# Performance work log

Measured on AMD Instinct MI355X. Metric: run time of the kernel, lower is better.

Reference implementation:

```python
import jax, jax.numpy as jnp
import numpy as np

B, N, C = 2, 2048, 1024
H = 16
D = C // H  # head_dim = 64
SCALE = D ** -0.5


def setup_inputs() -> dict:
    key = jax.random.key(0)
    k1, k2, k3, k4 = jax.random.split(key, 4)
    x = jax.random.normal(k1, (B, N, C), dtype=jnp.float32)
    # nn.Linear(in_dim, 3*out_dim, bias=False): store as [in, 3*out] for x @ W
    w_qkv = jax.random.normal(k2, (C, 3 * C), dtype=jnp.float32) * (C ** -0.5)
    w_proj = jax.random.normal(k3, (C, C), dtype=jnp.float32) * (C ** -0.5)
    b_proj = jax.random.normal(k4, (C,), dtype=jnp.float32) * 0.01
    return {"x": x, "w_qkv": w_qkv, "w_proj": w_proj, "b_proj": b_proj}


def reference(x, w_qkv, w_proj, b_proj):
    b, n, c = x.shape
    # QKV projection -> [3, B, H, N, D]
    qkv = (x @ w_qkv).reshape(b, n, 3, H, D).transpose(2, 0, 3, 1, 4)
    q, k, v = qkv[0], qkv[1], qkv[2]
    # scaled dot-product attention, full [B, H, N, N] scores as in original
    attn = jax.nn.softmax(jnp.einsum('bhqd,bhkd->bhqk', q * SCALE, k), axis=-1)
    out = jnp.einsum('bhqk,bhkd->bhqd', attn, v)  # [B, H, N, D]
    out = out.transpose(0, 2, 1, 3).reshape(b, n, c)
    return out @ w_proj + b_proj
```

## Files before the change

kernel.cpp:

```cpp
#include <hip/hip_runtime.h>

typedef unsigned short u16;
typedef float f32x4 __attribute__((ext_vector_type(4)));
typedef short bf16x8 __attribute__((ext_vector_type(8)));
typedef u16 u16x4 __attribute__((ext_vector_type(4)));
typedef u16 u16x8 __attribute__((ext_vector_type(8)));
typedef __bf16 bfr4 __attribute__((ext_vector_type(4)));

#define BB 2
#define NN 2048
#define CC 1024
#define HH 16
#define DD 64
#define MM (BB * NN)
#define NQKV (3 * CC)
#define QSCALE 0.18033688011112042f

#if __has_builtin(__builtin_amdgcn_exp2f)
#define EXP2(x) __builtin_amdgcn_exp2f(x)
#else
#define EXP2(x) exp2f(x)
#endif

__device__ __forceinline__ u16 f2bf(float f) {
    unsigned u = __float_as_uint(f);
    u += 0x7FFFu + ((u >> 16) & 1u);
    return (u16)(u >> 16);
}

__device__ __forceinline__ void ld_lds16(const u16* g, u16* l) {
    __builtin_amdgcn_global_load_lds(
        (const __attribute__((address_space(1))) unsigned int*)g,
        (__attribute__((address_space(3))) unsigned int*)l, 16, 0, 0);
}

__global__ __launch_bounds__(256) void k_prep(const float* __restrict__ x,
                                              const float* __restrict__ wqkv,
                                              const float* __restrict__ wproj,
                                              u16* __restrict__ Xb,
                                              u16* __restrict__ Wq,
                                              u16* __restrict__ Wp) {
    __shared__ float tile[32][33];
    int bid = blockIdx.x, t = threadIdx.x;
    if (bid < 2048) {
        int i = (bid * 256 + t) * 8;
        float4 a = *(const float4*)(x + i);
        float4 b = *(const float4*)(x + i + 4);
        u16x8 o;
        o[0] = f2bf(a.x); o[1] = f2bf(a.y); o[2] = f2bf(a.z); o[3] = f2bf(a.w);
        o[4] = f2bf(b.x); o[5] = f2bf(b.y); o[6] = f2bf(b.z); o[7] = f2bf(b.w);
        *(u16x8*)(Xb + i) = o;
        return;
    }
    const float* in;
    u16* out;
    int Nn, n0, k0;
    if (bid < 2048 + 3072) {
        int b2 = bid - 2048;
        in = wqkv; out = Wq; Nn = NQKV;
        n0 = (b2 % 96) * 32; k0 = (b2 / 96) * 32;
    } else {
        int b3 = bid - 5120;
        in = wproj; out = Wp; Nn = CC;
        n0 = (b3 & 31) * 32; k0 = (b3 >> 5) * 32;
    }
    int tx = t & 31, ty = t >> 5;
#pragma unroll
    for (int r = 0; r < 32; r += 8)
        tile[ty + r][tx] = in[(size_t)(k0 + ty + r) * Nn + n0 + tx];
    __syncthreads();
#pragma unroll
    for (int r = 0; r < 32; r += 8)
        out[(size_t)(n0 + ty + r) * CC + k0 + tx] = f2bf(tile[tx][ty + r]);
}

__global__ __launch_bounds__(512) void k_gemmq(
    const u16* __restrict__ A, const u16* __restrict__ B,
    u16* __restrict__ Qb, u16* __restrict__ Kb, u16* __restrict__ Vb) {
    const int Kd = 1024;
    __shared__ __align__(16) u16 Ah0[256][64], Bh0[256][64];
    __shared__ __align__(16) u16 Ah1[256][64], Bh1[256][64];

    int t = threadIdx.x, wave = t >> 6, lane = t & 63;
    int quad = lane >> 4, l16 = lane & 15;
    int wr = wave >> 2, wc = wave & 3;
    int m0 = blockIdx.y * 256, n0 = blockIdx.x * 256;

    int strow = wave * 8 + (lane >> 3);
    int stdst = (lane & 7) * 8;
    int stsrc = ((lane & 7) ^ (lane >> 3)) * 8;

    f32x4 acc[8][4];
#pragma unroll
    for (int i = 0; i < 8; i++)
#pragma unroll
        for (int j = 0; j < 4; j++) acc[i][j] = f32x4{0.f, 0.f, 0.f, 0.f};

    auto STAGE = [&](int k0, u16 (*Ad)[64], u16 (*Bd)[64]) {
#pragma unroll
        for (int i = 0; i < 4; i++) {
            int row = i * 64 + strow;
            ld_lds16(A + (size_t)(m0 + row) * Kd + k0 + stsrc, &Ad[row][stdst]);
            ld_lds16(B + (size_t)(n0 + row) * Kd + k0 + stsrc, &Bd[row][stdst]);
        }
    };
    auto COMPUTE = [&](u16 (*As)[64], u16 (*Bs)[64]) {
#pragma unroll
        for (int s = 0; s < 2; s++) {
            int pos = ((s * 4 + quad) ^ (l16 & 7)) * 8;
            bf16x8 af[8], bg[4];
#pragma unroll
            for (int m = 0; m < 8; m++)
                af[m] = *(const bf16x8*)&As[wr * 128 + m * 16 + l16][pos];
#pragma unroll
            for (int n = 0; n < 4; n++)
                bg[n] = *(const bf16x8*)&Bs[wc * 64 + n * 16 + l16][pos];
#pragma unroll
            for (int m = 0; m < 8; m++)
#pragma unroll
                for (int n = 0; n < 4; n++)
                    acc[m][n] = __builtin_amdgcn_mfma_f32_16x16x32_bf16(
                        af[m], bg[n], acc[m][n], 0, 0, 0);
        }
    };

    STAGE(0, Ah0, Bh0);
    __syncthreads();
    for (int k0 = 0; k0 < Kd; k0 += 128) {
        STAGE(k0 + 64, Ah1, Bh1);
        COMPUTE(Ah0, Bh0);
        __syncthreads();
        if (k0 + 128 < Kd) STAGE(k0 + 128, Ah0, Bh0);
        COMPUTE(Ah1, Bh1);
        __syncthreads();
    }

#pragma unroll
    for (int m = 0; m < 8; m++)
#pragma unroll
        for (int n = 0; n < 4; n++)
#pragma unroll
            for (int r = 0; r < 4; r++) {
                int grow = m0 + wr * 128 + m * 16 + quad * 4 + r;
                int gcol = n0 + wc * 64 + n * 16 + l16;
                float v = acc[m][n][r];
                int three = gcol >> 10, rem = gcol & 1023;
                int h = rem >> 6, d = rem & 63;
                int bb = grow >> 11, nn = grow & 2047;
                if (three == 0) {
                    Qb[((size_t)(bb * HH + h) * NN + nn) * DD + d] = f2bf(v * QSCALE);
                } else if (three == 1) {
                    Kb[((size_t)(bb * HH + h) * NN + nn) * DD + d] = f2bf(v);
                } else {
                    Vb[((size_t)(bb * HH + h) * DD + d) * NN + nn] = f2bf(v);
                }
            }
}

__global__ __launch_bounds__(256) void k_gemmp(
    const u16* __restrict__ A, const u16* __restrict__ B,
    const float* __restrict__ bias, float* __restrict__ Cout) {
    const int Kd = 1024;
    __shared__ __align__(16) u16 Ah[128][32];
    __shared__ __align__(16) u16 Bh[128][32];

    int t = threadIdx.x;
    int wave = t >> 6, lane = t & 63;
    int quad = lane >> 4, l16 = lane & 15;
    int wm = (wave >> 1) * 64, wn = (wave & 1) * 64;
    int m0 = blockIdx.y * 128, n0 = blockIdx.x * 128;

    int strow0 = wave * 16 + (lane >> 2);
    int stdst  = (lane & 3) * 8;
    int stsrc  = ((lane & 3) ^ ((lane >> 3) & 3)) * 8;
    int cfrag = (quad ^ ((l16 >> 1) & 3)) * 8;

    f32x4 acc[4][4];
#pragma unroll
    for (int i = 0; i < 4; i++)
#pragma unroll
        for (int j = 0; j < 4; j++) acc[i][j] = f32x4{0.f, 0.f, 0.f, 0.f};

    for (int k0 = 0; k0 < Kd; k0 += 32) {
        __syncthreads();
#pragma unroll
        for (int ii = 0; ii < 2; ii++) {
            int row = strow0 + ii * 64;
            ld_lds16(A + (size_t)(m0 + row) * Kd + k0 + stsrc, &Ah[row][stdst]);
            ld_lds16(B + (size_t)(n0 + row) * Kd + k0 + stsrc, &Bh[row][stdst]);
        }
        __syncthreads();

        bf16x8 af[4], bf[4];
#pragma unroll
        for (int i = 0; i < 4; i++) {
            af[i] = *(const bf16x8*)&Ah[wm + i * 16 + l16][cfrag];
            bf[i] = *(const bf16x8*)&Bh[wn + i * 16 + l16][cfrag];
        }
#pragma unroll
        for (int mi = 0; mi < 4; mi++)
#pragma unroll
            for (int ni = 0; ni < 4; ni++)
                acc[mi][ni] = __builtin_amdgcn_mfma_f32_16x16x32_bf16(
                    af[mi], bf[ni], acc[mi][ni], 0, 0, 0);
    }

#pragma unroll
    for (int mi = 0; mi < 4; mi++)
#pragma unroll
        for (int ni = 0; ni < 4; ni++)
#pragma unroll
            for (int r = 0; r < 4; r++) {
                int grow = m0 + wm + mi * 16 + quad * 4 + r;
                int gcol = n0 + wn + ni * 16 + l16;
                Cout[(size_t)grow * CC + gcol] = acc[mi][ni][r] + bias[gcol];
            }
}

__global__ __launch_bounds__(512) void k_attn(const u16* __restrict__ Qb,
                                              const u16* __restrict__ Kb,
                                              const u16* __restrict__ VbT,
                                              u16* __restrict__ Ob) {
    __shared__ __align__(16) u16 Ks0[64][64], Ks1[64][64];
    __shared__ __align__(16) u16 Vs0[64][64], Vs1[64][64];
    __shared__ __align__(16) u16 Ps[8][16][72];

    int t = threadIdx.x, wave = t >> 6, lane = t & 63;
    int quad = lane >> 4, l16 = lane & 15;
    int bh = blockIdx.y, q0 = blockIdx.x * 128;
    const size_t kbase = (size_t)bh * NN * DD;
    const size_t vbase = (size_t)bh * DD * NN;

    int qrow = q0 + wave * 16 + l16;
    bf16x8 qf0 = *(const bf16x8*)&Qb[kbase + (size_t)qrow * DD + quad * 8];
    bf16x8 qf1 = *(const bf16x8*)&Qb[kbase + (size_t)qrow * DD + 32 + quad * 8];

    f32x4 o[4];
#pragma unroll
    for (int i = 0; i < 4; i++) o[i] = f32x4{0.f, 0.f, 0.f, 0.f};
    f32x4 lrow = f32x4{0.f, 0.f, 0.f, 0.f};

    int stgrp = lane & 7;
    int stsrc = (stgrp ^ (lane >> 3)) * 8;
    int strow = wave * 8 + (lane >> 3);
    int cf0 = (quad ^ (l16 & 7)) * 8;
    int cf1 = ((4 + quad) ^ (l16 & 7)) * 8;

    auto STAGE = [&](int cc, u16 (*Kd_)[64], u16 (*Vd_)[64]) {
        ld_lds16(&Kb[kbase + (size_t)(cc * 64 + strow) * DD + stsrc],
                 &Kd_[strow][stgrp * 8]);
        ld_lds16(&VbT[vbase + (size_t)strow * NN + cc * 64 + stsrc],
                 &Vd_[strow][stgrp * 8]);
    };

    auto COMPUTE = [&](u16 (*Ksrc)[64], u16 (*Vsrc)[64]) {
        bf16x8 kf[4][2];
#pragma unroll
        for (int kt = 0; kt < 4; kt++) {
            kf[kt][0] = *(const bf16x8*)&Ksrc[kt * 16 + l16][cf0];
            kf[kt][1] = *(const bf16x8*)&Ksrc[kt * 16 + l16][cf1];
        }
        f32x4 s[4];
        __builtin_amdgcn_s_setprio(1);
#pragma unroll
        for (int kt = 0; kt < 4; kt++) {
            f32x4 z = f32x4{0.f, 0.f, 0.f, 0.f};
            z = __builtin_amdgcn_mfma_f32_16x16x32_bf16(kf[kt][0], qf0, z, 0, 0, 0);
            z = __builtin_amdgcn_mfma_f32_16x16x32_bf16(kf[kt][1], qf1, z, 0, 0, 0);
            s[kt] = z;
        }
        __builtin_amdgcn_s_setprio(0);
#pragma unroll
        for (int kt = 0; kt < 4; kt++) {
            bfr4 pk;
#pragma unroll
            for (int r = 0; r < 4; r++) {
                float e = EXP2(s[kt][r]);
                lrow[r] += e;
                pk[r] = (__bf16)e;
            }
            *(bfr4*)&Ps[wave][l16][kt * 16 + quad * 4] = pk;
        }
        __asm__ volatile("s_waitcnt lgkmcnt(0)" ::: "memory");
        bf16x8 pb0 = *(const bf16x8*)&Ps[wave][l16][quad * 8];
        bf16x8 pb1 = *(const bf16x8*)&Ps[wave][l16][32 + quad * 8];
        __builtin_amdgcn_s_setprio(1);
#pragma unroll
        for (int dt = 0; dt < 4; dt++) {
            bf16x8 vf0 = *(const bf16x8*)&Vsrc[dt * 16 + l16][cf0];
            bf16x8 vf1 = *(const bf16x8*)&Vsrc[dt * 16 + l16][cf1];
            o[dt] = __builtin_amdgcn_mfma_f32_16x16x32_bf16(vf0, pb0, o[dt], 0, 0, 0);
            o[dt] = __builtin_amdgcn_mfma_f32_16x16x32_bf16(vf1, pb1, o[dt], 0, 0, 0);
        }
        __builtin_amdgcn_s_setprio(0);
    };

    STAGE(0, Ks0, Vs0);
    __syncthreads();

    for (int c = 0; c < NN / 64; c += 2) {
        STAGE(c + 1, Ks1, Vs1);
        COMPUTE(Ks0, Vs0);
        __syncthreads();
        if (c + 2 < NN / 64) STAGE(c + 2, Ks0, Vs0);
        COMPUTE(Ks1, Vs1);
        __syncthreads();
    }

    int b = bh >> 4, h = bh & 15;
    float l = (lrow[0] + lrow[1]) + (lrow[2] + lrow[3]);
    l += __shfl_xor(l, 16, 64);
    l += __shfl_xor(l, 32, 64);
    float inv = 1.f / l;
    int grow = b * NN + q0 + wave * 16 + l16;
#pragma unroll
    for (int dt = 0; dt < 4; dt++) {
        u16x4 hv;
#pragma unroll
        for (int r = 0; r < 4; r++) hv[r] = f2bf(o[dt][r] * inv);
        int gcol = h * DD + dt * 16 + quad * 4;
        *(u16x4*)&Ob[(size_t)grow * CC + gcol] = hv;
    }
}

extern "C" void kernel_launch(void* const* d_in, const int* in_sizes, int n_in,
                              void* d_out, int out_size, void* d_ws, size_t ws_size,
                              hipStream_t stream) {
    const float* x      = (const float*)d_in[0];
    const float* w_qkv  = (const float*)d_in[1];
    const float* w_proj = (const float*)d_in[2];
    const float* b_proj = (const float*)d_in[3];
    float* out = (float*)d_out;

    u16* p = (u16*)d_ws;
    u16* Xb = p; p += (size_t)MM * CC;
    u16* Wq = p; p += (size_t)NQKV * CC;
    u16* Wp = p; p += (size_t)CC * CC;
    u16* Qb = p; p += (size_t)MM * CC;
    u16* Kb = p; p += (size_t)MM * CC;
    u16* Vb = p; p += (size_t)MM * CC;
    u16* Ob = p; p += (size_t)MM * CC;

    k_prep<<<2048 + 3072 + 1024, 256, 0, stream>>>(x, w_qkv, w_proj, Xb, Wq, Wp);
    k_gemmq<<<dim3(NQKV / 256, MM / 256), 512, 0, stream>>>(Xb, Wq, Qb, Kb, Vb);
    k_attn<<<dim3(NN / 128, BB * HH), 512, 0, stream>>>(Qb, Kb, Vb, Ob);
    k_gemmp<<<dim3(CC / 128, MM / 128), 256, 0, stream>>>(Ob, Wp, b_proj, out);
}
```

Baseline: 203.4 us.

## Shrink GEMM tiles for more blocks, double-buffer projection GEMM, raise MFMA priority

The QKV GEMM moves from 256x256 to 128x192 tiles, which turns 192 blocks into 512 so the 256 CUs get better occupancy and wave balance. The output-projection GEMM is rewritten from a single-buffered 128x128, K=32 loop into a double-buffered 64x128, K=64 pipeline with the swizzled staging, giving 512 blocks. Both kernels raise wave priority around their MFMA bursts. The cost is lower per-block data reuse, so each block loads more operand bytes from global memory per output.

```diff
diff --git a/kernel.cpp b/kernel.cpp
--- a/kernel.cpp
+++ b/kernel.cpp
@@ -74,33 +74,37 @@
         out[(size_t)(n0 + ty + r) * CC + k0 + tx] = f2bf(tile[tx][ty + r]);
 }
 
-__global__ __launch_bounds__(512) void k_gemmq(
+__global__ __launch_bounds__(512, 4) void k_gemmq(
     const u16* __restrict__ A, const u16* __restrict__ B,
     u16* __restrict__ Qb, u16* __restrict__ Kb, u16* __restrict__ Vb) {
     const int Kd = 1024;
-    __shared__ __align__(16) u16 Ah0[256][64], Bh0[256][64];
-    __shared__ __align__(16) u16 Ah1[256][64], Bh1[256][64];
+    __shared__ __align__(16) u16 Ah0[128][64], Bh0[192][64];
+    __shared__ __align__(16) u16 Ah1[128][64], Bh1[192][64];
 
     int t = threadIdx.x, wave = t >> 6, lane = t & 63;
     int quad = lane >> 4, l16 = lane & 15;
     int wr = wave >> 2, wc = wave & 3;
-    int m0 = blockIdx.y * 256, n0 = blockIdx.x * 256;
+    int m0 = blockIdx.y * 128, n0 = blockIdx.x * 192;
 
     int strow = wave * 8 + (lane >> 3);
     int stdst = (lane & 7) * 8;
     int stsrc = ((lane & 7) ^ (lane >> 3)) * 8;
 
-    f32x4 acc[8][4];
-#pragma unroll
-    for (int i = 0; i < 8; i++)
-#pragma unroll
-        for (int j = 0; j < 4; j++) acc[i][j] = f32x4{0.f, 0.f, 0.f, 0.f};
+    f32x4 acc[4][3];
+#pragma unroll
+    for (int i = 0; i < 4; i++)
+#pragma unroll
+        for (int j = 0; j < 3; j++) acc[i][j] = f32x4{0.f, 0.f, 0.f, 0.f};
 
     auto STAGE = [&](int k0, u16 (*Ad)[64], u16 (*Bd)[64]) {
 #pragma unroll
-        for (int i = 0; i < 4; i++) {
+        for (int i = 0; i < 2; i++) {
             int row = i * 64 + strow;
             ld_lds16(A + (size_t)(m0 + row) * Kd + k0 + stsrc, &Ad[row][stdst]);
+        }
+#pragma unroll
+        for (int i = 0; i < 3; i++) {
+            int row = i * 64 + strow;
             ld_lds16(B + (size_t)(n0 + row) * Kd + k0 + stsrc, &Bd[row][stdst]);
         }
     };
@@ -108,19 +112,21 @@
 #pragma unroll
         for (int s = 0; s < 2; s++) {
             int pos = ((s * 4 + quad) ^ (l16 & 7)) * 8;
-            bf16x8 af[8], bg[4];
-#pragma unroll
-            for (int m = 0; m < 8; m++)
-                af[m] = *(const bf16x8*)&As[wr * 128 + m * 16 + l16][pos];
-#pragma unroll
-            for (int n = 0; n < 4; n++)
-                bg[n] = *(const bf16x8*)&Bs[wc * 64 + n * 16 + l16][pos];
-#pragma unroll
-            for (int m = 0; m < 8; m++)
-#pragma unroll
-                for (int n = 0; n < 4; n++)
+            bf16x8 af[4], bg[3];
+#pragma unroll
+            for (int m = 0; m < 4; m++)
+                af[m] = *(const bf16x8*)&As[wr * 64 + m * 16 + l16][pos];
+#pragma unroll
+            for (int n = 0; n < 3; n++)
+                bg[n] = *(const bf16x8*)&Bs[wc * 48 + n * 16 + l16][pos];
+            __builtin_amdgcn_s_setprio(1);
+#pragma unroll
+            for (int m = 0; m < 4; m++)
+#pragma unroll
+                for (int n = 0; n < 3; n++)
                     acc[m][n] = __builtin_amdgcn_mfma_f32_16x16x32_bf16(
                         af[m], bg[n], acc[m][n], 0, 0, 0);
+            __builtin_amdgcn_s_setprio(0);
         }
     };
 
@@ -136,13 +142,13 @@
     }
 
 #pragma unroll
-    for (int m = 0; m < 8; m++)
-#pragma unroll
-        for (int n = 0; n < 4; n++)
+    for (int m = 0; m < 4; m++)
+#pragma unroll
+        for (int n = 0; n < 3; n++)
 #pragma unroll
             for (int r = 0; r < 4; r++) {
-                int grow = m0 + wr * 128 + m * 16 + quad * 4 + r;
-                int gcol = n0 + wc * 64 + n * 16 + l16;
+                int grow = m0 + wr * 64 + m * 16 + quad * 4 + r;
+                int gcol = n0 + wc * 48 + n * 16 + l16;
                 float v = acc[m][n][r];
                 int three = gcol >> 10, rem = gcol & 1023;
                 int h = rem >> 6, d = rem & 63;
@@ -161,59 +167,77 @@
     const u16* __restrict__ A, const u16* __restrict__ B,
     const float* __restrict__ bias, float* __restrict__ Cout) {
     const int Kd = 1024;
-    __shared__ __align__(16) u16 Ah[128][32];
-    __shared__ __align__(16) u16 Bh[128][32];
-
-    int t = threadIdx.x;
-    int wave = t >> 6, lane = t & 63;
+    __shared__ __align__(16) u16 Ah0[64][64], Bh0[128][64];
+    __shared__ __align__(16) u16 Ah1[64][64], Bh1[128][64];
+
+    int t = threadIdx.x, wave = t >> 6, lane = t & 63;
     int quad = lane >> 4, l16 = lane & 15;
-    int wm = (wave >> 1) * 64, wn = (wave & 1) * 64;
-    int m0 = blockIdx.y * 128, n0 = blockIdx.x * 128;
-
-    int strow0 = wave * 16 + (lane >> 2);
-    int stdst  = (lane & 3) * 8;
-    int stsrc  = ((lane & 3) ^ ((lane >> 3) & 3)) * 8;
-    int cfrag = (quad ^ ((l16 >> 1) & 3)) * 8;
-
-    f32x4 acc[4][4];
+    int m0 = blockIdx.y * 64, n0 = blockIdx.x * 128;
+
+    int strow = wave * 8 + (lane >> 3);
+    int stdst = (lane & 7) * 8;
+    int stsrc = ((lane & 7) ^ (lane >> 3)) * 8;
+
+    f32x4 acc[4][2];
 #pragma unroll
     for (int i = 0; i < 4; i++)
 #pragma unroll
-        for (int j = 0; j < 4; j++) acc[i][j] = f32x4{0.f, 0.f, 0.f, 0.f};
-
-    for (int k0 = 0; k0 < Kd; k0 += 32) {
-        __syncthreads();
-#pragma unroll
-        for (int ii = 0; ii < 2; ii++) {
-            int row = strow0 + ii * 64;
-            ld_lds16(A + (size_t)(m0 + row) * Kd + k0 + stsrc, &Ah[row][stdst]);
-            ld_lds16(B + (size_t)(n0 + row) * Kd + k0 + stsrc, &Bh[row][stdst]);
-        }
-        __syncthreads();
-
-        bf16x8 af[4], bf[4];
+        for (int j = 0; j < 2; j++) acc[i][j] = f32x4{0.f, 0.f, 0.f, 0.f};
+
+    auto STAGE = [&](int k0, u16 (*Ad)[64], u16 (*Bd)[64]) {
+#pragma unroll
+        for (int i = 0; i < 2; i++) {
+            int row = i * 32 + strow;
+            ld_lds16(A + (size_t)(m0 + row) * Kd + k0 + stsrc, &Ad[row][stdst]);
+        }
 #pragma unroll
         for (int i = 0; i < 4; i++) {
-            af[i] = *(const bf16x8*)&Ah[wm + i * 16 + l16][cfrag];
-            bf[i] = *(const bf16x8*)&Bh[wn + i * 16 + l16][cfrag];
-        }
-#pragma unroll
-        for (int mi = 0; mi < 4; mi++)
-#pragma unroll
-            for (int ni = 0; ni < 4; ni++)
-                acc[mi][ni] = __builtin_amdgcn_mfma_f32_16x16x32_bf16(
-                    af[mi], bf[ni], acc[mi][ni], 0, 0, 0);
-    }
-
-#pragma unroll
-    for (int mi = 0; mi < 4; mi++)
-#pragma unroll
-        for (int ni = 0; ni < 4; ni++)
+            int row = i * 32 + strow;
+            ld_lds16(B + (size_t)(n0 + row) * Kd + k0 + stsrc, &Bd[row][stdst]);
+        }
+    };
+    auto COMPUTE = [&](u16 (*As)[64], u16 (*Bs)[64]) {
+#pragma unroll
+        for (int s = 0; s < 2; s++) {
+            int pos = ((s * 4 + quad) ^ (l16 & 7)) * 8;
+            bf16x8 af[4], bg[2];
+#pragma unroll
+            for (int m = 0; m < 4; m++)
+                af[m] = *(const bf16x8*)&As[m * 16 + l16][pos];
+#pragma unroll
+            for (int n = 0; n < 2; n++)
+                bg[n] = *(const bf16x8*)&Bs[wave * 32 + n * 16 + l16][pos];
+            __builtin_amdgcn_s_setprio(1);
+#pragma unroll
+            for (int m = 0; m < 4; m++)
+#pragma unroll
+                for (int n = 0; n < 2; n++)
+                    acc[m][n] = __builtin_amdgcn_mfma_f32_16x16x32_bf16(
+                        af[m], bg[n], acc[m][n], 0, 0, 0);
+            __builtin_amdgcn_s_setprio(0);
+        }
+    };
+
+    STAGE(0, Ah0, Bh0);
+    __syncthreads();
+    for (int k0 = 0; k0 < Kd; k0 += 128) {
+        STAGE(k0 + 64, Ah1, Bh1);
+        COMPUTE(Ah0, Bh0);
+        __syncthreads();
+        if (k0 + 128 < Kd) STAGE(k0 + 128, Ah0, Bh0);
+        COMPUTE(Ah1, Bh1);
+        __syncthreads();
+    }
+
+#pragma unroll
+    for (int m = 0; m < 4; m++)
+#pragma unroll
+        for (int n = 0; n < 2; n++)
 #pragma unroll
             for (int r = 0; r < 4; r++) {
-                int grow = m0 + wm + mi * 16 + quad * 4 + r;
-                int gcol = n0 + wn + ni * 16 + l16;
-                Cout[(size_t)grow * CC + gcol] = acc[mi][ni][r] + bias[gcol];
+                int grow = m0 + m * 16 + quad * 4 + r;
+                int gcol = n0 + wave * 32 + n * 16 + l16;
+                Cout[(size_t)grow * CC + gcol] = acc[m][n][r] + bias[gcol];
             }
 }
 
@@ -342,7 +366,7 @@
     u16* Ob = p; p += (size_t)MM * CC;
 
     k_prep<<<2048 + 3072 + 1024, 256, 0, stream>>>(x, w_qkv, w_proj, Xb, Wq, Wp);
-    k_gemmq<<<dim3(NQKV / 256, MM / 256), 512, 0, stream>>>(Xb, Wq, Qb, Kb, Vb);
+    k_gemmq<<<dim3(NQKV / 192, MM / 128), 512, 0, stream>>>(Xb, Wq, Qb, Kb, Vb);
     k_attn<<<dim3(NN / 128, BB * HH), 512, 0, stream>>>(Qb, Kb, Vb, Ob);
-    k_gemmp<<<dim3(CC / 128, MM / 128), 256, 0, stream>>>(Ob, Wp, b_proj, out);
-}
+    k_gemmp<<<dim3(CC / 128, MM / 64), 256, 0, stream>>>(Ob, Wp, b_proj, out);
+}
```

Result: faster. 195.5 us (-3.9%).
